# Kernel optimization log

Hardware: AMD Instinct MI355X
Metric: run time of the kernel (lower is better)

Reference implementation:

```python
import jax, jax.numpy as jnp
import numpy as np

B, T, D = 4, 2048, 1024  # batch, seq_len, dec_dim_in == dim_proj_QK == dim_proj_V == dec_dim_out


def setup_inputs() -> dict:
    key = jax.random.key(0)
    ks = jax.random.split(key, 9)
    s = 1.0 / np.sqrt(D)  # torch Linear default init scale
    return {
        "x": jax.random.normal(ks[0], (B, T, D), dtype=jnp.float32),
        "Wq": jax.random.uniform(ks[1], (D, D), jnp.float32, -s, s),
        "bq": jax.random.uniform(ks[2], (D,), jnp.float32, -s, s),
        "Wk": jax.random.uniform(ks[3], (D, D), jnp.float32, -s, s),
        "bk": jax.random.uniform(ks[4], (D,), jnp.float32, -s, s),
        "Wv": jax.random.uniform(ks[5], (D, D), jnp.float32, -s, s),
        "bv": jax.random.uniform(ks[6], (D,), jnp.float32, -s, s),
        "Wh": jax.random.uniform(ks[7], (D, D), jnp.float32, -s, s),
        "bh": jax.random.uniform(ks[8], (D,), jnp.float32, -s, s),
    }


def reference(x, Wq, bq, Wk, bk, Wv, bv, Wh, bh):
    Q = x @ Wq + bq                      # [B, T, Dqk]
    K = x @ Wk + bk                      # [B, T, Dqk]
    V = x @ Wv + bv                      # [B, T, Dv]
    scale = 1.0 / jnp.sqrt(jnp.asarray(K.shape[-1], x.dtype))
    scores = jnp.einsum("btd,bsd->bts", Q, K) * scale  # [B, T, T]
    t = K.shape[1]
    causal = jnp.triu(jnp.ones((t, t), dtype=bool), k=1)  # True above diagonal
    scores = jnp.where(causal[None, :, :], -jnp.inf, scores)
    attn = jax.nn.softmax(scores, axis=-1)
    # dropout is identity in eval mode (reference baseline)
    out = jnp.einsum("bts,bsd->btd", attn, V)  # [B, T, Dv]
    return out @ Wh + bh
```

## Files before the change

### kernel.cpp

```cpp
#include <hip/hip_runtime.h>


typedef __attribute__((ext_vector_type(8)))  short short8;
typedef __attribute__((ext_vector_type(4)))  float f4;

#define BM 128
#define BN 128
#define BK 64
#define BM2 256
#define BN2 256

#define F_OBF    1
#define F_SKIP   2
#define F_KLIM   4
#define F_REVY   8
#define F_VSPL   16
#define F_RSCL   32
#define F_EXP    64
#define F_RSUM   128
#define F_SPLITK 256

#define WAITV4() asm volatile("s_waitcnt vmcnt(4)" ::: "memory")
#define WAITV8() asm volatile("s_waitcnt vmcnt(8)" ::: "memory")
#define WAITV0() asm volatile("s_waitcnt vmcnt(0)" ::: "memory")
#define SBAR()   __builtin_amdgcn_s_barrier()
#define PRIO1()  __builtin_amdgcn_s_setprio(1)
#define PRIO0()  __builtin_amdgcn_s_setprio(0)

__device__ inline unsigned short f2bf(float f) {
    union { float f; unsigned u; } c; c.f = f;
    unsigned u = c.u;
    return (unsigned short)((u + 0x7fffu + ((u >> 16) & 1u)) >> 16);
}
__device__ inline float bf2f(unsigned short u) {
    union { unsigned u; float f; } c; c.u = ((unsigned)u) << 16;
    return c.f;
}
__device__ inline void gload16(const void* g, void* l) {
    __builtin_amdgcn_global_load_lds(
        (const __attribute__((address_space(1))) void*)g,
        (__attribute__((address_space(3))) void*)l,
        16, 0, 0);
}

template<int FLAGS>
__global__ __launch_bounds__(256)
void gemm_bt(const unsigned short* __restrict__ A,
             const unsigned short* __restrict__ Bt,
             void* __restrict__ C,
             const float* __restrict__ bias,
             int M, int N, int K, int lda, int ldb, int ldc,
             long sA, long sB, long sC,
             float scale,
             unsigned short* __restrict__ C2, long sC2, int Tv, int vsplit,
             float* __restrict__ rowsums)
{
    const int b = blockIdx.z;
    A  += (long)b * sA;
    Bt += (long)b * sB;

    int by = blockIdx.y;
    if (FLAGS & F_REVY) by = gridDim.y - 1 - by;
    const int m0 = by * BM;
    const int n0 = blockIdx.x * BN;

    const int kt1 = K / BK;

    __shared__ unsigned short As[BM * BK];
    __shared__ unsigned short Bs[BN * BK];

    const int tid  = threadIdx.x;
    const int lane = tid & 63;
    const int wave = tid >> 6;
    const int wm   = wave & 1;
    const int wn   = wave >> 1;
    const int lrow = lane & 15;
    const int quad = lane >> 4;

    f4 acc[4][4];
#pragma unroll
    for (int i = 0; i < 4; ++i)
#pragma unroll
        for (int j = 0; j < 4; ++j) acc[i][j] = (f4)0.0f;

    const int srow = tid >> 3;
    const int gco  = ((tid & 7) ^ (srow & 7)) << 3;
    const int rdsl = (lrow & 7);

    for (int kt = 0; kt < kt1; ++kt) {
        const int k0 = kt * BK;
#pragma unroll
        for (int d = 0; d < 4; ++d) {
            const int row = d * 32 + srow;
            const unsigned short* ga = A  + (long)(m0 + row) * lda + k0 + gco;
            const unsigned short* gb = Bt + (long)(n0 + row) * ldb + k0 + gco;
            const int ldsoff = (d * 256 + wave * 64) * 16;
            gload16(ga, (char*)As + ldsoff);
            gload16(gb, (char*)Bs + ldsoff);
        }
        __syncthreads();

#pragma unroll
        for (int ks = 0; ks < 2; ++ks) {
            const int slot = ((ks * 4 + quad) ^ rdsl) << 3;
            short8 af[4], bfr[4];
#pragma unroll
            for (int i = 0; i < 4; ++i) {
                af[i]  = *(const short8*)(As + (wm * 64 + i * 16 + lrow) * BK + slot);
                bfr[i] = *(const short8*)(Bs + (wn * 64 + i * 16 + lrow) * BK + slot);
            }
#pragma unroll
            for (int i = 0; i < 4; ++i)
#pragma unroll
                for (int j = 0; j < 4; ++j)
                    acc[i][j] = __builtin_amdgcn_mfma_f32_16x16x32_bf16(
                        af[i], bfr[j], acc[i][j], 0, 0, 0);
        }
        __syncthreads();
    }

    const int row0 = m0 + wm * 64 + quad * 4;
    const int col0 = n0 + wn * 64 + lrow;

    float bj[4];
#pragma unroll
    for (int j = 0; j < 4; ++j) bj[j] = bias ? bias[col0 + j * 16] : 0.0f;

    unsigned short* Cb = (unsigned short*)C;
    float*          Cf = (float*)C;
    const long cbase = (long)b * sC;

#pragma unroll
    for (int i = 0; i < 4; ++i) {
#pragma unroll
        for (int j = 0; j < 4; ++j) {
            const int col = col0 + j * 16;
#pragma unroll
            for (int r = 0; r < 4; ++r) {
                const int row = row0 + i * 16 + r;
                float v = acc[i][j][r] * scale + bj[j];
                const long off = cbase + (long)row * ldc + col;
                if (FLAGS & F_OBF) Cb[off] = f2bf(v);
                else               Cf[off] = v;
            }
        }
    }
}

template<int HA>
__device__ inline void lda_half(short8 (&af)[8], const unsigned short* Asb,
                                int wm, int lrow, int quad, int rdsl)
{
#pragma unroll
    for (int i = 0; i < 4; ++i)
#pragma unroll
        for (int ks = 0; ks < 2; ++ks)
            af[i * 2 + ks] = *(const short8*)(
                Asb + (wm * 128 + HA * 64 + i * 16 + lrow) * BK
                    + (((ks * 4 + quad) ^ rdsl) << 3));
}

template<int QB>
__device__ inline void ldb_q(short8 (&bq)[4], const unsigned short* Bsb,
                             int wn, int lrow, int quad, int rdsl)
{
#pragma unroll
    for (int j = 0; j < 2; ++j)
#pragma unroll
        for (int ks = 0; ks < 2; ++ks)
            bq[j * 2 + ks] = *(const short8*)(
                Bsb + (wn * 64 + QB * 32 + j * 16 + lrow) * BK
                    + (((ks * 4 + quad) ^ rdsl) << 3));
}

template<int RI, int CJ>
__device__ inline void mfma_cl(f4 (&acc)[8][4], const short8 (&a)[8],
                               const short8 (&b)[4])
{
#pragma unroll
    for (int ks = 0; ks < 2; ++ks)
#pragma unroll
        for (int i = 0; i < 4; ++i)
#pragma unroll
            for (int j = 0; j < 2; ++j)
                acc[RI + i][CJ + j] = __builtin_amdgcn_mfma_f32_16x16x32_bf16(
                    a[i * 2 + ks], b[j * 2 + ks], acc[RI + i][CJ + j], 0, 0, 0);
}

__device__ inline void stage_mat(const unsigned short* __restrict__ Row,
                                 int k0, unsigned short* Ls, int ld, int tid)
{
    const int srow = tid >> 3;
    const int gco  = ((tid & 7) ^ (srow & 7)) << 3;
    const int wave = tid >> 6;
#pragma unroll
    for (int d = 0; d < 4; ++d) {
        const int row = d * 64 + srow;
        const int ldsoff = (d * 512 + wave * 64) * 16;
        gload16(Row + (long)row * ld + k0 + gco, (char*)Ls + ldsoff);
    }
}

template<int FLAGS, int GX = 0, int GY = 0>
__global__ __launch_bounds__(512)
void gemm256(const unsigned short* __restrict__ A,
             const unsigned short* __restrict__ Bt,
             void* __restrict__ C,
             const float* __restrict__ bias,
             int M, int N, int K, int lda, int ldb, int ldc,
             long sA, long sB, long sC,
             float scale,
             unsigned short* __restrict__ C2, long sC2, int Tv, int vsplit,
             float* __restrict__ rowsums)
{
    const int b = blockIdx.z;
    A  += (long)b * sA;
    Bt += (long)b * sB;
    if (FLAGS & (F_RSCL | F_RSUM)) rowsums += (long)b * M;

    int bxr = blockIdx.x, byr = blockIdx.y;
    if (GX > 0) {
        constexpr int NWG = GX * GY;
        constexpr int Q   = NWG >> 3;
        static_assert((NWG & 7) == 0, "swizzle needs NWG%8==0");
        const int lin  = byr * GX + bxr;
        const int virt = (lin & 7) * Q + (lin >> 3);
        bxr = virt % GX; byr = virt / GX;
    }

    int by = byr;
    if (FLAGS & F_REVY) by = gridDim.y - 1 - by;
    const int m0 = by * BM2;

    int n0, split = 0;
    if (FLAGS & F_SPLITK) {
        const int nbx = N / BN2;
        n0 = (bxr % nbx) * BN2;
        split = bxr / nbx;
        if (split && m0 < 1024) return;
    } else {
        n0 = bxr * BN2;
    }

    if ((FLAGS & F_SKIP) && n0 > m0 + (BM2 - 1)) return;

    int kend = K;
    if (FLAGS & F_KLIM) { int ke = m0 + BM2; kend = ke < K ? ke : K; }
    int kt0 = 0;
    if (FLAGS & F_SPLITK) {
        if (split == 0) { if (kend > 1024) kend = 1024; }
        else            { kt0 = 1024 / BK; }
    }
    const int kt1 = kend / BK;

    __shared__ unsigned short sm[4][BM2 * BK];

    const int tid  = threadIdx.x;
    const int lane = tid & 63;
    const int wave = tid >> 6;
    const int wm   = wave & 1;
    const int wn   = wave >> 1;
    const int lrow = lane & 15;
    const int quad = lane >> 4;
    const int rdsl = lrow & 7;

    f4 acc[8][4];
#pragma unroll
    for (int i = 0; i < 8; ++i)
#pragma unroll
        for (int j = 0; j < 4; ++j) acc[i][j] = (f4)0.0f;

    const unsigned short* Arow = A  + (long)m0 * lda;
    const unsigned short* Brow = Bt + (long)n0 * ldb;
    const int ktiles = kt1 - kt0;

    short8 af[8], bg0[4], bg1[4];

    stage_mat(Arow, kt0 * BK, sm[0], lda, tid);
    stage_mat(Brow, kt0 * BK, sm[1], ldb, tid);
    stage_mat(Arow, (kt0 + 1) * BK, sm[2], lda, tid);
    stage_mat(Brow, (kt0 + 1) * BK, sm[3], ldb, tid);
    WAITV8();
    SBAR();
    lda_half<0>(af, sm[0], wm, lrow, quad, rdsl);
    ldb_q<0>(bg0, sm[1], wn, lrow, quad, rdsl);

    for (int t = 0; t < ktiles; ++t) {
        const int cur = t & 1;
        const unsigned short* Asb = sm[cur * 2];
        const unsigned short* Bsb = sm[cur * 2 + 1];
        const bool s2 = (t + 2 < ktiles);
        const bool rd = (t + 1 < ktiles);

        PRIO1(); mfma_cl<0, 0>(acc, af, bg0); PRIO0();
        ldb_q<1>(bg1, Bsb, wn, lrow, quad, rdsl);

        PRIO1(); mfma_cl<0, 2>(acc, af, bg1); PRIO0();
        lda_half<1>(af, Asb, wm, lrow, quad, rdsl);
        SBAR();

        PRIO1(); mfma_cl<4, 2>(acc, af, bg1); PRIO0();
        if (s2) { stage_mat(Arow, (kt0 + t + 2) * BK, sm[cur * 2], lda, tid);
                  WAITV4(); }
        else    { WAITV0(); }
        SBAR();

        if (s2) stage_mat(Brow, (kt0 + t + 2) * BK, sm[cur * 2 + 1], ldb, tid);
        PRIO1(); mfma_cl<4, 0>(acc, af, bg0); PRIO0();
        if (rd) {
            const unsigned short* An = sm[(cur ^ 1) * 2];
            const unsigned short* Bn = sm[(cur ^ 1) * 2 + 1];
            lda_half<0>(af, An, wm, lrow, quad, rdsl);
            ldb_q<0>(bg0, Bn, wn, lrow, quad, rdsl);
        }
    }

    const int row0 = m0 + wm * 128 + quad * 4;
    const int col0 = n0 + wn * 64 + lrow;

    float bj[4];
#pragma unroll
    for (int j = 0; j < 4; ++j) bj[j] = bias ? bias[col0 + j * 16] : 0.0f;

    if ((FLAGS & F_VSPL) && n0 >= vsplit) {
        const int bidx  = m0 >> 11;
        const int tloc0 = (m0 & 2047) + wm * 128 + quad * 4;
#pragma unroll
        for (int j = 0; j < 4; ++j) {
            const int d = col0 + j * 16 - vsplit;
            unsigned short* base = C2 + (long)bidx * sC2 + (long)d * Tv;
#pragma unroll
            for (int i = 0; i < 8; ++i) {
                const int tt = tloc0 + i * 16;
                unsigned long long pk = 0;
#pragma unroll
                for (int r = 0; r < 4; ++r) {
                    float v = acc[i][j][r] * scale + bj[j];
                    pk |= (unsigned long long)f2bf(v) << (16 * r);
                }
                *(unsigned long long*)(base + tt) = pk;
            }
        }
        return;
    }

    float inv[32];
    if (FLAGS & F_RSCL) {
#pragma unroll
        for (int i = 0; i < 8; ++i)
#pragma unroll
            for (int r = 0; r < 4; ++r)
                inv[i * 4 + r] = rowsums[row0 + i * 16 + r];
    }

    float rs[32];
    if (FLAGS & F_RSUM) {
#pragma unroll
        for (int k = 0; k < 32; ++k) rs[k] = 0.0f;
    }

    unsigned short* Cb = (unsigned short*)C;
    float*          Cf = ((FLAGS & F_SPLITK) && split) ? (float*)C2 : (float*)C;
    const long cbase = (long)b * sC;

#pragma unroll
    for (int i = 0; i < 8; ++i) {
#pragma unroll
        for (int j = 0; j < 4; ++j) {
            const int col = col0 + j * 16;
#pragma unroll
            for (int r = 0; r < 4; ++r) {
                const int row = row0 + i * 16 + r;
                float v = acc[i][j][r] * scale;
                if (FLAGS & F_EXP) { v = __expf(v); if (col > row) v = 0.0f; }
                if (FLAGS & F_RSUM) rs[i * 4 + r] += v;
                if (FLAGS & F_RSCL) v *= inv[i * 4 + r];
                if (!((FLAGS & F_SPLITK) && split)) v += bj[j];
                const long off = cbase + (long)row * ldc + col;
                if (FLAGS & F_OBF) Cb[off] = f2bf(v);
                else               Cf[off] = v;
            }
        }
    }

    if (FLAGS & F_RSUM) {
#pragma unroll
        for (int k = 0; k < 32; ++k) {
            rs[k] += __shfl_xor(rs[k], 1);
            rs[k] += __shfl_xor(rs[k], 2);
            rs[k] += __shfl_xor(rs[k], 4);
            rs[k] += __shfl_xor(rs[k], 8);
        }
        if (lrow == 0) {
#pragma unroll
            for (int i = 0; i < 8; ++i)
#pragma unroll
                for (int r = 0; r < 4; ++r)
                    atomicAdd(&rowsums[row0 + i * 16 + r], rs[i * 4 + r]);
        }
    }
}

__global__ void combine_upper(float* __restrict__ out,
                              const float* __restrict__ part)
{
    const long base = ((long)blockIdx.y * 2048 + 1024) * 1024 / 4;
    const long i = base + blockIdx.x * 256 + threadIdx.x;
    f4 a = ((f4*)out)[i];
    f4 bb = ((const f4*)part)[i];
    a.x += bb.x; a.y += bb.y; a.z += bb.z; a.w += bb.w;
    ((f4*)out)[i] = a;
}

__global__ void recip_sums(float* __restrict__ s)
{
    const int i = blockIdx.x * 256 + threadIdx.x;
    s[i] = 1.0f / s[i];
}

__global__ void gemv_bhh(const unsigned short* __restrict__ Wht,
                         const float* __restrict__ bv,
                         const float* __restrict__ bh,
                         float* __restrict__ bhh)
{
    const int m = blockIdx.x;
    const int tid = threadIdx.x;
    const int lane = tid & 63, wave = tid >> 6;
    __shared__ float red[4];
    const unsigned short* row = Wht + (long)m * 1024;
    float s = 0.0f;
#pragma unroll
    for (int k = 0; k < 4; ++k) {
        const int idx = tid * 4 + k;
        s += bf2f(row[idx]) * bv[idx];
    }
    for (int o = 32; o > 0; o >>= 1) s += __shfl_down(s, o);
    if (lane == 0) red[wave] = s;
    __syncthreads();
    if (tid == 0) bhh[m] = red[0] + red[1] + red[2] + red[3] + bh[m];
}

__global__ void prep(const float* __restrict__ x,
                     const float* __restrict__ Wq, const float* __restrict__ Wk,
                     const float* __restrict__ Wv, const float* __restrict__ Wh,
                     const float* __restrict__ bq, const float* __restrict__ bk,
                     unsigned short* __restrict__ Xbf,
                     unsigned short* __restrict__ Wqkvt,
                     unsigned short* __restrict__ Wht,
                     unsigned short* __restrict__ Wvb,
                     float* __restrict__ bqkv)
{
    __shared__ unsigned short tsh[32][33];
    const int bid = blockIdx.x;
    const int tid = threadIdx.x;

    if (bid < 8192) {
        const int i = bid * 256 + tid;
        f4 v = ((const f4*)x)[i];
        unsigned long long p = (unsigned long long)f2bf(v.x)
                             | ((unsigned long long)f2bf(v.y) << 16)
                             | ((unsigned long long)f2bf(v.z) << 32)
                             | ((unsigned long long)f2bf(v.w) << 48);
        ((unsigned long long*)Xbf)[i] = p;
    } else if (bid < 9216) {
        const int i = (bid - 8192) * 256 + tid;
        f4 v = ((const f4*)Wv)[i];
        unsigned long long p = (unsigned long long)f2bf(v.x)
                             | ((unsigned long long)f2bf(v.y) << 16)
                             | ((unsigned long long)f2bf(v.z) << 32)
                             | ((unsigned long long)f2bf(v.w) << 48);
        ((unsigned long long*)Wvb)[i] = p;
    } else if (bid < 12288) {
        const int wi = bid - 9216;
        const int w = wi >> 10, tile = wi & 1023;
        const float* src = (w == 0) ? Wq : (w == 1) ? Wk : Wh;
        unsigned short* dst = (w == 0) ? Wqkvt : (w == 1) ? (Wqkvt + 1024 * 1024) : Wht;
        const int c0 = (tile & 31) * 32, r0 = (tile >> 5) * 32;
        const int xx = tid & 31, yy = tid >> 5;
        for (int i = yy; i < 32; i += 8)
            tsh[i][xx] = f2bf(src[(long)(r0 + i) * 1024 + c0 + xx]);
        __syncthreads();
        for (int i = yy; i < 32; i += 8)
            dst[(long)(c0 + i) * 1024 + r0 + xx] = tsh[xx][i];
    } else {
        const int i = (bid - 12288) * 256 + tid;
        if (i < 1024) { bqkv[i] = bq[i]; bqkv[1024 + i] = bk[i]; bqkv[2048 + i] = 0.0f; }
    }
}

extern "C" void kernel_launch(void* const* d_in, const int* in_sizes, int n_in,
                              void* d_out, int out_size, void* d_ws, size_t ws_size,
                              hipStream_t stream)
{
    const float* x  = (const float*)d_in[0];
    const float* Wq = (const float*)d_in[1];
    const float* bq = (const float*)d_in[2];
    const float* Wk = (const float*)d_in[3];
    const float* bk = (const float*)d_in[4];
    const float* Wv = (const float*)d_in[5];
    const float* bv = (const float*)d_in[6];
    const float* Wh = (const float*)d_in[7];
    const float* bh = (const float*)d_in[8];
    float* out = (float*)d_out;

    const int  Bb = 4, T = 2048, Dm = 1024;
    const long BT = (long)Bb * T;

    unsigned short* ws = (unsigned short*)d_ws;
    size_t o = 0;
    unsigned short* Xbf   = ws + o; o += (size_t)BT * Dm;
    unsigned short* Wqkvt = ws + o; o += (size_t)3 * Dm * Dm;
    unsigned short* Wht   = ws + o; o += (size_t)Dm * Dm;
    unsigned short* Wvb   = ws + o; o += (size_t)Dm * Dm;
    float* bqkv = (float*)(ws + o); o += (size_t)3 * Dm * 2;
    float* bhh  = (float*)(ws + o); o += (size_t)Dm * 2;
    float* sums = (float*)(ws + o); o += (size_t)BT * 2;
    unsigned short* QKV   = ws + o; o += (size_t)BT * 3 * Dm;
    unsigned short* Vt    = ws + o; o += (size_t)BT * Dm;
    unsigned short* Pp    = ws + o; o += (size_t)Bb * T * T;
    float* part = (float*)(ws + o);

    const dim3 blk(256);
    const dim3 blk2(512);
    const long sRow3 = (long)T * 3 * Dm;

    hipMemsetAsync(sums, 0, (size_t)BT * sizeof(float), stream);

    prep<<<12289, blk, 0, stream>>>(x, Wq, Wk, Wv, Wh, bq, bk,
                                    Xbf, Wqkvt, Wht, Wvb, bqkv);

    gemm_bt<F_OBF><<<dim3(Dm / BN, Dm / BM, 1), blk, 0, stream>>>(
        Wht, Wvb, Wqkvt + 2 * Dm * Dm, nullptr, Dm, Dm, Dm, Dm, Dm, Dm,
        0, 0, 0, 1.0f, nullptr, 0, 0, 0, nullptr);

    gemv_bhh<<<Dm, blk, 0, stream>>>(Wht, bv, bh, bhh);

    gemm256<F_OBF | F_VSPL, 12, 32>
        <<<dim3(3 * Dm / BN2, BT / BM2, 1), blk2, 0, stream>>>(
        Xbf, Wqkvt, QKV, bqkv, (int)BT, 3 * Dm, Dm, Dm, Dm, 3 * Dm,
        0, 0, 0, 1.0f, Vt, (long)Dm * T, T, 2 * Dm, nullptr);

    gemm256<F_OBF | F_SKIP | F_REVY | F_EXP | F_RSUM>
        <<<dim3(T / BN2, T / BM2, Bb), blk2, 0, stream>>>(
        QKV, QKV + Dm, Pp, nullptr, T, T, Dm, 3 * Dm, 3 * Dm, T,
        sRow3, sRow3, (long)T * T, 1.0f / 32.0f,
        nullptr, 0, 0, 0, sums);

    recip_sums<<<dim3((int)(BT / 256)), blk, 0, stream>>>(sums);

    gemm256<F_KLIM | F_REVY | F_RSCL | F_SPLITK, 8, 8>
        <<<dim3(2 * Dm / BN2, T / BM2, Bb), blk2, 0, stream>>>(
        Pp, Vt, out, bhh, T, Dm, T, T, T, Dm,
        (long)T * T, (long)Dm * T, (long)T * Dm, 1.0f,
        (unsigned short*)part, 0, 0, 0, sums);

    combine_upper<<<dim3(1024, Bb), blk, 0, stream>>>(out, part);
}
```

Measured before the change: 279.5 us.

## Shrink wide GEMM tiles to 128x256 with a simplified double-buffered pipeline

Replaces the 256x256 GEMM tile with a 128x256 tile: each of the 8 waves now holds a 64x64 accumulator block instead of 128x64, A staging is halved, and the main loop is reduced to two MFMA phases with A and B tiles staged together. The grids double in the M dimension, with matching swizzle parameters, for the QKV projection, the causal score GEMM and the PV GEMM. This aims to raise occupancy and cut register pressure, and to make causal skipping and K-limiting finer-grained. The cost is less data reuse per tile and more global/LDS traffic per FLOP.

```diff
diff --git a/kernel.cpp b/kernel.cpp
--- a/kernel.cpp
+++ b/kernel.cpp
@@ -7,8 +7,8 @@
 #define BM 128
 #define BN 128
 #define BK 64
-#define BM2 256
-#define BN2 256
+#define BM3 128
+#define BN3 256
 
 #define F_OBF    1
 #define F_SKIP   2
@@ -20,7 +20,7 @@
 #define F_RSUM   128
 #define F_SPLITK 256
 
-#define WAITV4() asm volatile("s_waitcnt vmcnt(4)" ::: "memory")
+#define WAITV6() asm volatile("s_waitcnt vmcnt(6)" ::: "memory")
 #define WAITV8() asm volatile("s_waitcnt vmcnt(8)" ::: "memory")
 #define WAITV0() asm volatile("s_waitcnt vmcnt(0)" ::: "memory")
 #define SBAR()   __builtin_amdgcn_s_barrier()
@@ -147,16 +147,15 @@
     }
 }
 
-template<int HA>
-__device__ inline void lda_half(short8 (&af)[8], const unsigned short* Asb,
-                                int wm, int lrow, int quad, int rdsl)
+__device__ inline void lda_w(short8 (&af)[8], const unsigned short* Asb,
+                             int wm, int lrow, int quad, int rdsl)
 {
 #pragma unroll
     for (int i = 0; i < 4; ++i)
 #pragma unroll
         for (int ks = 0; ks < 2; ++ks)
             af[i * 2 + ks] = *(const short8*)(
-                Asb + (wm * 128 + HA * 64 + i * 16 + lrow) * BK
+                Asb + (wm * 64 + i * 16 + lrow) * BK
                     + (((ks * 4 + quad) ^ rdsl) << 3));
 }
 
@@ -173,9 +172,9 @@
                     + (((ks * 4 + quad) ^ rdsl) << 3));
 }
 
-template<int RI, int CJ>
-__device__ inline void mfma_cl(f4 (&acc)[8][4], const short8 (&a)[8],
-                               const short8 (&b)[4])
+template<int CJ>
+__device__ inline void mfma16(f4 (&acc)[4][4], const short8 (&a)[8],
+                              const short8 (&b)[4])
 {
 #pragma unroll
     for (int ks = 0; ks < 2; ++ks)
@@ -183,10 +182,11 @@
         for (int i = 0; i < 4; ++i)
 #pragma unroll
             for (int j = 0; j < 2; ++j)
-                acc[RI + i][CJ + j] = __builtin_amdgcn_mfma_f32_16x16x32_bf16(
-                    a[i * 2 + ks], b[j * 2 + ks], acc[RI + i][CJ + j], 0, 0, 0);
-}
-
+                acc[i][CJ + j] = __builtin_amdgcn_mfma_f32_16x16x32_bf16(
+                    a[i * 2 + ks], b[j * 2 + ks], acc[i][CJ + j], 0, 0, 0);
+}
+
+template<int ND>
 __device__ inline void stage_mat(const unsigned short* __restrict__ Row,
                                  int k0, unsigned short* Ls, int ld, int tid)
 {
@@ -194,7 +194,7 @@
     const int gco  = ((tid & 7) ^ (srow & 7)) << 3;
     const int wave = tid >> 6;
 #pragma unroll
-    for (int d = 0; d < 4; ++d) {
+    for (int d = 0; d < ND; ++d) {
         const int row = d * 64 + srow;
         const int ldsoff = (d * 512 + wave * 64) * 16;
         gload16(Row + (long)row * ld + k0 + gco, (char*)Ls + ldsoff);
@@ -203,15 +203,15 @@
 
 template<int FLAGS, int GX = 0, int GY = 0>
 __global__ __launch_bounds__(512)
-void gemm256(const unsigned short* __restrict__ A,
-             const unsigned short* __restrict__ Bt,
-             void* __restrict__ C,
-             const float* __restrict__ bias,
-             int M, int N, int K, int lda, int ldb, int ldc,
-             long sA, long sB, long sC,
-             float scale,
-             unsigned short* __restrict__ C2, long sC2, int Tv, int vsplit,
-             float* __restrict__ rowsums)
+void gemmw(const unsigned short* __restrict__ A,
+           const unsigned short* __restrict__ Bt,
+           void* __restrict__ C,
+           const float* __restrict__ bias,
+           int M, int N, int K, int lda, int ldb, int ldc,
+           long sA, long sB, long sC,
+           float scale,
+           unsigned short* __restrict__ C2, long sC2, int Tv, int vsplit,
+           float* __restrict__ rowsums)
 {
     const int b = blockIdx.z;
     A  += (long)b * sA;
@@ -230,22 +230,22 @@
 
     int by = byr;
     if (FLAGS & F_REVY) by = gridDim.y - 1 - by;
-    const int m0 = by * BM2;
+    const int m0 = by * BM3;
 
     int n0, split = 0;
     if (FLAGS & F_SPLITK) {
-        const int nbx = N / BN2;
-        n0 = (bxr % nbx) * BN2;
+        const int nbx = N / BN3;
+        n0 = (bxr % nbx) * BN3;
         split = bxr / nbx;
         if (split && m0 < 1024) return;
     } else {
-        n0 = bxr * BN2;
-    }
-
-    if ((FLAGS & F_SKIP) && n0 > m0 + (BM2 - 1)) return;
+        n0 = bxr * BN3;
+    }
+
+    if ((FLAGS & F_SKIP) && n0 > m0 + (BM3 - 1)) return;
 
     int kend = K;
-    if (FLAGS & F_KLIM) { int ke = m0 + BM2; kend = ke < K ? ke : K; }
+    if (FLAGS & F_KLIM) { int ke = m0 + BM3; kend = ke < K ? ke : K; }
     int kt0 = 0;
     if (FLAGS & F_SPLITK) {
         if (split == 0) { if (kend > 1024) kend = 1024; }
@@ -253,7 +253,8 @@
     }
     const int kt1 = kend / BK;
 
-    __shared__ unsigned short sm[4][BM2 * BK];
+    __shared__ unsigned short smA[2][BM3 * BK];
+    __shared__ unsigned short smB[2][BN3 * BK];
 
     const int tid  = threadIdx.x;
     const int lane = tid & 63;
@@ -264,9 +265,9 @@
     const int quad = lane >> 4;
     const int rdsl = lrow & 7;
 
-    f4 acc[8][4];
-#pragma unroll
-    for (int i = 0; i < 8; ++i)
+    f4 acc[4][4];
+#pragma unroll
+    for (int i = 0; i < 4; ++i)
 #pragma unroll
         for (int j = 0; j < 4; ++j) acc[i][j] = (f4)0.0f;
 
@@ -276,46 +277,40 @@
 
     short8 af[8], bg0[4], bg1[4];
 
-    stage_mat(Arow, kt0 * BK, sm[0], lda, tid);
-    stage_mat(Brow, kt0 * BK, sm[1], ldb, tid);
-    stage_mat(Arow, (kt0 + 1) * BK, sm[2], lda, tid);
-    stage_mat(Brow, (kt0 + 1) * BK, sm[3], ldb, tid);
-    WAITV8();
+    stage_mat<2>(Arow, kt0 * BK, smA[0], lda, tid);
+    stage_mat<4>(Brow, kt0 * BK, smB[0], ldb, tid);
+    stage_mat<2>(Arow, (kt0 + 1) * BK, smA[1], lda, tid);
+    stage_mat<4>(Brow, (kt0 + 1) * BK, smB[1], ldb, tid);
+    WAITV6();
     SBAR();
-    lda_half<0>(af, sm[0], wm, lrow, quad, rdsl);
-    ldb_q<0>(bg0, sm[1], wn, lrow, quad, rdsl);
+    lda_w(af, smA[0], wm, lrow, quad, rdsl);
+    ldb_q<0>(bg0, smB[0], wn, lrow, quad, rdsl);
 
     for (int t = 0; t < ktiles; ++t) {
         const int cur = t & 1;
-        const unsigned short* Asb = sm[cur * 2];
-        const unsigned short* Bsb = sm[cur * 2 + 1];
         const bool s2 = (t + 2 < ktiles);
         const bool rd = (t + 1 < ktiles);
 
-        PRIO1(); mfma_cl<0, 0>(acc, af, bg0); PRIO0();
-        ldb_q<1>(bg1, Bsb, wn, lrow, quad, rdsl);
-
-        PRIO1(); mfma_cl<0, 2>(acc, af, bg1); PRIO0();
-        lda_half<1>(af, Asb, wm, lrow, quad, rdsl);
+        PRIO1(); mfma16<0>(acc, af, bg0); PRIO0();
+        ldb_q<1>(bg1, smB[cur], wn, lrow, quad, rdsl);
         SBAR();
 
-        PRIO1(); mfma_cl<4, 2>(acc, af, bg1); PRIO0();
-        if (s2) { stage_mat(Arow, (kt0 + t + 2) * BK, sm[cur * 2], lda, tid);
-                  WAITV4(); }
-        else    { WAITV0(); }
+        PRIO1(); mfma16<2>(acc, af, bg1); PRIO0();
+        if (s2) {
+            stage_mat<2>(Arow, (kt0 + t + 2) * BK, smA[cur], lda, tid);
+            stage_mat<4>(Brow, (kt0 + t + 2) * BK, smB[cur], ldb, tid);
+            WAITV6();
+        } else {
+            WAITV0();
+        }
         SBAR();
-
-        if (s2) stage_mat(Brow, (kt0 + t + 2) * BK, sm[cur * 2 + 1], ldb, tid);
-        PRIO1(); mfma_cl<4, 0>(acc, af, bg0); PRIO0();
         if (rd) {
-            const unsigned short* An = sm[(cur ^ 1) * 2];
-            const unsigned short* Bn = sm[(cur ^ 1) * 2 + 1];
-            lda_half<0>(af, An, wm, lrow, quad, rdsl);
-            ldb_q<0>(bg0, Bn, wn, lrow, quad, rdsl);
-        }
-    }
-
-    const int row0 = m0 + wm * 128 + quad * 4;
+            lda_w(af, smA[cur ^ 1], wm, lrow, quad, rdsl);
+            ldb_q<0>(bg0, smB[cur ^ 1], wn, lrow, quad, rdsl);
+        }
+    }
+
+    const int row0 = m0 + wm * 64 + quad * 4;
     const int col0 = n0 + wn * 64 + lrow;
 
     float bj[4];
@@ -324,13 +319,13 @@
 
     if ((FLAGS & F_VSPL) && n0 >= vsplit) {
         const int bidx  = m0 >> 11;
-        const int tloc0 = (m0 & 2047) + wm * 128 + quad * 4;
+        const int tloc0 = (m0 & 2047) + wm * 64 + quad * 4;
 #pragma unroll
         for (int j = 0; j < 4; ++j) {
             const int d = col0 + j * 16 - vsplit;
             unsigned short* base = C2 + (long)bidx * sC2 + (long)d * Tv;
 #pragma unroll
-            for (int i = 0; i < 8; ++i) {
+            for (int i = 0; i < 4; ++i) {
                 const int tt = tloc0 + i * 16;
                 unsigned long long pk = 0;
 #pragma unroll
@@ -344,19 +339,19 @@
         return;
     }
 
-    float inv[32];
+    float inv[16];
     if (FLAGS & F_RSCL) {
 #pragma unroll
-        for (int i = 0; i < 8; ++i)
+        for (int i = 0; i < 4; ++i)
 #pragma unroll
             for (int r = 0; r < 4; ++r)
                 inv[i * 4 + r] = rowsums[row0 + i * 16 + r];
     }
 
-    float rs[32];
+    float rs[16];
     if (FLAGS & F_RSUM) {
 #pragma unroll
-        for (int k = 0; k < 32; ++k) rs[k] = 0.0f;
+        for (int k = 0; k < 16; ++k) rs[k] = 0.0f;
     }
 
     unsigned short* Cb = (unsigned short*)C;
@@ -364,7 +359,7 @@
     const long cbase = (long)b * sC;
 
 #pragma unroll
-    for (int i = 0; i < 8; ++i) {
+    for (int i = 0; i < 4; ++i) {
 #pragma unroll
         for (int j = 0; j < 4; ++j) {
             const int col = col0 + j * 16;
@@ -385,7 +380,7 @@
 
     if (FLAGS & F_RSUM) {
 #pragma unroll
-        for (int k = 0; k < 32; ++k) {
+        for (int k = 0; k < 16; ++k) {
             rs[k] += __shfl_xor(rs[k], 1);
             rs[k] += __shfl_xor(rs[k], 2);
             rs[k] += __shfl_xor(rs[k], 4);
@@ -393,7 +388,7 @@
         }
         if (lrow == 0) {
 #pragma unroll
-            for (int i = 0; i < 8; ++i)
+            for (int i = 0; i < 4; ++i)
 #pragma unroll
                 for (int r = 0; r < 4; ++r)
                     atomicAdd(&rowsums[row0 + i * 16 + r], rs[i * 4 + r]);
@@ -535,21 +530,21 @@
 
     gemv_bhh<<<Dm, blk, 0, stream>>>(Wht, bv, bh, bhh);
 
-    gemm256<F_OBF | F_VSPL, 12, 32>
-        <<<dim3(3 * Dm / BN2, BT / BM2, 1), blk2, 0, stream>>>(
+    gemmw<F_OBF | F_VSPL, 12, 64>
+        <<<dim3(3 * Dm / BN3, BT / BM3, 1), blk2, 0, stream>>>(
         Xbf, Wqkvt, QKV, bqkv, (int)BT, 3 * Dm, Dm, Dm, Dm, 3 * Dm,
         0, 0, 0, 1.0f, Vt, (long)Dm * T, T, 2 * Dm, nullptr);
 
-    gemm256<F_OBF | F_SKIP | F_REVY | F_EXP | F_RSUM>
-        <<<dim3(T / BN2, T / BM2, Bb), blk2, 0, stream>>>(
+    gemmw<F_OBF | F_SKIP | F_REVY | F_EXP | F_RSUM, 8, 16>
+        <<<dim3(T / BN3, T / BM3, Bb), blk2, 0, stream>>>(
         QKV, QKV + Dm, Pp, nullptr, T, T, Dm, 3 * Dm, 3 * Dm, T,
         sRow3, sRow3, (long)T * T, 1.0f / 32.0f,
         nullptr, 0, 0, 0, sums);
 
     recip_sums<<<dim3((int)(BT / 256)), blk, 0, stream>>>(sums);
 
-    gemm256<F_KLIM | F_REVY | F_RSCL | F_SPLITK, 8, 8>
-        <<<dim3(2 * Dm / BN2, T / BM2, Bb), blk2, 0, stream>>>(
+    gemmw<F_KLIM | F_REVY | F_RSCL | F_SPLITK, 8, 16>
+        <<<dim3(2 * Dm / BN3, T / BM3, Bb), blk2, 0, stream>>>(
         Pp, Vt, out, bhh, T, Dm, T, T, T, Dm,
         (long)T * T, (long)Dm * T, (long)T * Dm, 1.0f,
         (unsigned short*)part, 0, 0, 0, sums);
```

Result: slower. 314.7 us (+12.6%).
